# Kernel tuning notes

Measured on AMD Instinct MI355X. Metric: run time of the kernel, lower is better.

Reference implementation:

```python
import jax, jax.numpy as jnp
import numpy as np

NUM_HEADS = 16
D_MODEL = 2048
DUPLICATES = 4
DEPTH = D_MODEL // NUM_HEADS  # 128
KV_HEADS = NUM_HEADS // DUPLICATES  # 4


def rope(x):
    # x: (b, s, d); RoPE over first 2*(d//2) dims (d even here), as in source
    b, s, d = x.shape
    dim = d // 2
    inv_freq = (10000.0 ** (-jnp.arange(0, dim, dtype=jnp.float32) / dim)).astype(x.dtype)
    pos = jnp.arange(s, dtype=x.dtype)[None, :, None]  # (1, s, 1)
    freqs = pos * inv_freq  # (1, s, dim)
    cos, sin = jnp.cos(freqs), jnp.sin(freqs)
    x1, x2 = x[..., :dim], x[..., dim:]
    return jnp.concatenate([x1 * cos - x2 * sin, x2 * cos + x1 * sin], axis=-1)


def setup_inputs() -> dict:
    key = jax.random.key(0)
    ks = jax.random.split(key, 6)
    b, s = 2, 2048
    x = jax.random.normal(ks[0], (b, s, D_MODEL), dtype=jnp.float32)
    mask = jnp.ones((b, 1, s, s), dtype=bool)
    std = 0.02
    Wq = jax.random.normal(ks[1], (D_MODEL, D_MODEL), dtype=jnp.float32) * std
    Wk = jax.random.normal(ks[2], (D_MODEL, D_MODEL // DUPLICATES), dtype=jnp.float32) * std
    Wv = jax.random.normal(ks[3], (D_MODEL, D_MODEL // DUPLICATES), dtype=jnp.float32) * std
    Wo = jax.random.normal(ks[4], (D_MODEL, D_MODEL), dtype=jnp.float32) * std
    bo = jnp.zeros((1, 1, D_MODEL), dtype=jnp.float32)
    return {"x": x, "mask": mask, "Wq": Wq, "Wk": Wk, "Wv": Wv, "Wo": Wo, "bo": bo}


def reference(x, mask, Wq, Wk, Wv, Wo, bo):
    b, s, d = x.shape
    # QKV projections; RoPE applied on full projected vectors (as in source)
    q = rope(x @ Wq)          # (b, s, d_model)
    k = rope(x @ Wk)          # (b, s, d_model/dup)
    v = x @ Wv                # (b, s, d_model/dup)
    # split heads
    q = q.reshape(b, s, NUM_HEADS, DEPTH).transpose(0, 2, 1, 3)     # (b, H, s, depth)
    k = k.reshape(b, s, KV_HEADS, DEPTH).transpose(0, 2, 1, 3)      # (b, Hkv, s, depth)
    v = v.reshape(b, s, KV_HEADS, DEPTH).transpose(0, 2, 1, 3)
    # GQA repeat (jnp.repeat on head axis, matching source)
    k = jnp.repeat(k, DUPLICATES, axis=1)                            # (b, H, s, depth)
    v = jnp.repeat(v, DUPLICATES, axis=1)
    # scaled dot-product attention (chunking in source is a pure partition of q; math identical)
    logits = jnp.einsum('bhqd,bhkd->bhqk', q, k) / jnp.sqrt(jnp.asarray(DEPTH, x.dtype))
    logits = jnp.where(mask, logits, jnp.asarray(-1e9, x.dtype))
    attn = jax.nn.softmax(logits, axis=-1)
    out = jnp.einsum('bhqk,bhkd->bhqd', attn, v)                     # (b, H, s, depth)
    out = out.transpose(0, 2, 1, 3).reshape(b, s, d)
    return out @ Wo + bo
```

## Files before the change

kernel.cpp:

```cpp
#include <hip/hip_runtime.h>
#include <hip/hip_bf16.h>
#include <stdint.h>

#define NHEADS 16
#define KVHEADS 4
#define DEPTH 128
#define SEQ 2048
#define DM 2048
#define NQKV 3072
#define SCALE 0.08838834764831845f

using u16 = unsigned short;
using u32 = unsigned int;
using u64 = unsigned long long;
using bf16x8 = __attribute__((ext_vector_type(8))) __bf16;
using f32x4  = __attribute__((ext_vector_type(4))) float;
using f32x16 = __attribute__((ext_vector_type(16))) float;
using u32x4  = __attribute__((ext_vector_type(4))) u32;

__device__ __forceinline__ u16 bits(float f) {
  return __builtin_bit_cast(u16, (__bf16)f);
}
__device__ __forceinline__ u32 pk2(float a, float b) {
  return (u32)bits(a) | ((u32)bits(b) << 16);
}

__device__ __forceinline__ void gll16(const void* g, void* l) {
  __builtin_amdgcn_global_load_lds((const __attribute__((address_space(1))) void*)g,
                                   (__attribute__((address_space(3))) void*)l, 16, 0, 0);
}


__global__ void k_cvt_x(const float4* __restrict__ x, u16* __restrict__ o, int n4) {
  int i = blockIdx.x * 256 + threadIdx.x;
  if (i >= n4) return;
  float4 v = x[i];
  u64 pk = (u64)bits(v.x) | ((u64)bits(v.y) << 16) | ((u64)bits(v.z) << 32) | ((u64)bits(v.w) << 48);
  reinterpret_cast<u64*>(o)[i] = pk;
}

__global__ void k_transpose_w(const float* __restrict__ in, u16* __restrict__ out, int K, int N) {
  __shared__ float tile[32][33];
  int n0 = blockIdx.x * 32, k0 = blockIdx.y * 32;
  int tx = threadIdx.x, ty = threadIdx.y;
  for (int i = 0; i < 4; i++) tile[ty + i * 8][tx] = in[(size_t)(k0 + ty + i * 8) * N + n0 + tx];
  __syncthreads();
  for (int i = 0; i < 4; i++)
    out[(size_t)(n0 + ty + i * 8) * K + k0 + tx] = bits(tile[tx][ty + i * 8]);
}

__global__ void k_trig(float2* __restrict__ tab) {
  int idx = blockIdx.x * 256 + threadIdx.x;
  int s = idx >> 10, j = idx & 1023;
  float inv = expf((float)j * (-9.210340371976184f / 1024.f));
  float f = (float)s * inv;
  float sv, cv;
  sincosf(f, &sv, &cv);
  tab[idx] = make_float2(cv, sv);
}

__global__ void k_rope_q(const float* __restrict__ qkv, const float2* __restrict__ tab,
                         u16* __restrict__ Qh) {
  int idx = blockIdx.x * 256 + threadIdx.x;
  int col = idx & 2047;
  int row = idx >> 11;
  int s = row & 2047;
  const float* base = qkv + (size_t)row * NQKV;
  float v = base[col], out;
  if (col < 1024) {
    float2 cs = tab[s * 1024 + col];
    out = v * cs.x - base[col + 1024] * cs.y;
  } else {
    int j = col - 1024;
    float2 cs = tab[s * 1024 + j];
    out = v * cs.x + base[col - 1024] * cs.y;
  }
  int h = col >> 7, d = col & 127;
  Qh[(((size_t)(row >> 11) * NHEADS + h) * SEQ + s) * DEPTH + d] = bits(out * SCALE);
}

__global__ void k_rope_k(const float* __restrict__ qkv, const float2* __restrict__ tab,
                         u16* __restrict__ Kh) {
  int idx = blockIdx.x * 256 + threadIdx.x;
  int col = idx & 511;
  int row = idx >> 9;
  int s = row & 2047;
  const float* base = qkv + (size_t)row * NQKV + 2048;
  float v = base[col], out;
  if (col < 256) {
    float2 cs = tab[s * 1024 + col * 4];
    out = v * cs.x - base[col + 256] * cs.y;
  } else {
    int j = col - 256;
    float2 cs = tab[s * 1024 + j * 4];
    out = v * cs.x + base[col - 256] * cs.y;
  }
  int h = col >> 7, d = col & 127;
  Kh[(((size_t)(row >> 11) * KVHEADS + h) * SEQ + s) * DEPTH + d] = bits(out);
}

__global__ void k_transpose_v(const float* __restrict__ qkv, u16* __restrict__ Vt) {
  __shared__ float tile[32][33];
  int gy = blockIdx.y;
  int d0 = (gy & 3) * 32, kvh = (gy >> 2) & 3, b = gy >> 4;
  int s0 = blockIdx.x * 32;
  int tx = threadIdx.x, ty = threadIdx.y;
  const float* base = qkv + (size_t)b * SEQ * NQKV + 2560 + kvh * 128 + d0;
  for (int i = 0; i < 4; i++)
    tile[ty + i * 8][tx] = base[(size_t)(s0 + ty + i * 8) * NQKV + tx];
  __syncthreads();
  u16* obase = Vt + (((size_t)b * KVHEADS + kvh) * DEPTH + d0) * SEQ;
  for (int i = 0; i < 4; i++)
    obase[(size_t)(ty + i * 8) * SEQ + s0 + tx] = bits(tile[tx][ty + i * 8]);
}


#define GBAR __builtin_amdgcn_s_barrier()

#define GSTAGE(GBASE, LHALF, KT, ROWB) do {                                   \
  _Pragma("unroll") for (int i_ = 0; i_ < 2; i_++) {                          \
    int rl_ = (l >> 3) + w * 8 + i_ * 64;                                     \
    int cs_ = (l & 7) ^ ((rl_ & 4) >> 1);                                     \
    gll16((GBASE) + (size_t)((ROWB) + rl_) * K + (KT) * 64 + cs_ * 8,         \
          (char*)(LHALF) + w * 1024 + i_ * 8192);                             \
  }                                                                           \
} while (0)

#define LDA8(DB, MH) do {                                                     \
  const char* pa_ = (const char*)lA[DB][wm];                                  \
  _Pragma("unroll") for (int mi_ = 0; mi_ < 4; mi_++)                         \
  _Pragma("unroll") for (int kk_ = 0; kk_ < 2; kk_++) {                       \
    int row_ = (MH) * 64 + mi_ * 16 + lr;                                     \
    af[mi_ * 2 + kk_] = *(const bf16x8*)(pa_ + row_ * 128 +                   \
        (((kk_ * 4 + lg) ^ ((row_ & 4) >> 1)) * 16));                         \
  }                                                                           \
} while (0)

#define LDB4(DB, NH) do {                                                     \
  const char* pb_ = (const char*)lB[DB][wn >> 1];                             \
  _Pragma("unroll") for (int ni_ = 0; ni_ < 2; ni_++)                         \
  _Pragma("unroll") for (int kk_ = 0; kk_ < 2; kk_++) {                       \
    int row_ = (wn & 1) * 64 + (NH) * 32 + ni_ * 16 + lr;                     \
    bfr[ni_ * 2 + kk_] = *(const bf16x8*)(pb_ + row_ * 128 +                  \
        (((kk_ * 4 + lg) ^ ((row_ & 4) >> 1)) * 16));                         \
  }                                                                           \
} while (0)

#define PHASE_MFMA(MH, NH) do {                                               \
  __builtin_amdgcn_s_setprio(1);                                             \
  _Pragma("unroll") for (int mi_ = 0; mi_ < 4; mi_++)                         \
  _Pragma("unroll") for (int ni_ = 0; ni_ < 2; ni_++)                         \
  _Pragma("unroll") for (int kk_ = 0; kk_ < 2; kk_++)                         \
    acc[MH][NH][mi_][ni_] = __builtin_amdgcn_mfma_f32_16x16x32_bf16(          \
        af[mi_ * 2 + kk_], bfr[ni_ * 2 + kk_], acc[MH][NH][mi_][ni_], 0, 0, 0); \
  __builtin_amdgcn_s_setprio(0);                                             \
} while (0)

__global__ __launch_bounds__(512, 2) void k_gemm256(const u16* __restrict__ A,
                                                    const u16* __restrict__ B,
                                                    float* __restrict__ C, int M, int N, int K,
                                                    const float* __restrict__ bias) {
  __shared__ __align__(16) u16 lA[2][2][128 * 64];
  __shared__ __align__(16) u16 lB[2][2][128 * 64];
  int nt = N >> 8;
  int nwg = gridDim.x;
  int bid = blockIdx.x;
  int swz = (bid & 7) * (nwg >> 3) + (bid >> 3);
  int bm = swz / nt, bn = swz % nt;
  int tid = threadIdx.x;
  int w = tid >> 6, l = tid & 63;
  int lr = l & 15, lg = l >> 4;
  int wm = w >> 2, wn = w & 3;
  const u16* Abase = A + (size_t)(bm * 256) * K;
  const u16* Bbase = B + (size_t)(bn * 256) * K;
  int NT = K >> 6;

  f32x4 acc[2][2][4][2] = {};

  GSTAGE(Abase, lA[0][0], 0, 0);
  GSTAGE(Abase, lA[0][1], 0, 128);
  GSTAGE(Bbase, lB[0][0], 0, 0);
  GSTAGE(Bbase, lB[0][1], 0, 128);
  GSTAGE(Abase, lA[1][0], 1, 0);
  asm volatile("s_waitcnt vmcnt(2)" ::: "memory");
  GBAR;

  for (int j = 0; j < (NT >> 1); j++) {
    int kt1 = 2 * j + 1;
    int ktn0 = (2 * j + 2) & (NT - 1);
    int ktn1 = (2 * j + 3) & (NT - 1);
    bf16x8 af[8];
    bf16x8 bfr[4];
    LDA8(0, 0);
    LDB4(0, 0);
    GSTAGE(Abase, lA[1][1], kt1, 128);
    GBAR;
    PHASE_MFMA(0, 0);
    GBAR;
    LDB4(0, 1);
    GSTAGE(Bbase, lB[1][0], kt1, 0);
    GBAR;
    PHASE_MFMA(0, 1);
    GBAR;
    LDA8(0, 1);
    GSTAGE(Bbase, lB[1][1], kt1, 128);
    GBAR;
    PHASE_MFMA(1, 1);
    GBAR;
    LDB4(0, 0);
    GSTAGE(Abase, lA[0][0], ktn0, 0);
    asm volatile("s_waitcnt vmcnt(2)" ::: "memory");
    GBAR;
    PHASE_MFMA(1, 0);
    GBAR;
    LDA8(1, 0);
    LDB4(1, 0);
    GSTAGE(Abase, lA[0][1], ktn0, 128);
    GBAR;
    PHASE_MFMA(0, 0);
    GBAR;
    LDB4(1, 1);
    GSTAGE(Bbase, lB[0][0], ktn0, 0);
    GBAR;
    PHASE_MFMA(0, 1);
    GBAR;
    LDA8(1, 1);
    GSTAGE(Bbase, lB[0][1], ktn0, 128);
    GBAR;
    PHASE_MFMA(1, 1);
    GBAR;
    LDB4(1, 0);
    GSTAGE(Abase, lA[1][0], ktn1, 0);
    asm volatile("s_waitcnt vmcnt(2)" ::: "memory");
    GBAR;
    PHASE_MFMA(1, 0);
    GBAR;
  }
  asm volatile("s_waitcnt vmcnt(0)" ::: "memory");

  int r0 = bm * 256 + wm * 128, c0 = bn * 256 + wn * 64;
#pragma unroll
  for (int mh = 0; mh < 2; mh++)
#pragma unroll
    for (int mi = 0; mi < 4; mi++)
#pragma unroll
      for (int nh = 0; nh < 2; nh++)
#pragma unroll
        for (int ni = 0; ni < 2; ni++) {
          int col = c0 + nh * 32 + ni * 16 + lr;
          float bv = bias ? bias[col] : 0.f;
#pragma unroll
          for (int r = 0; r < 4; r++) {
            int row = r0 + mh * 64 + mi * 16 + lg * 4 + r;
            C[(size_t)row * N + col] = acc[mh][nh][mi][ni][r] + bv;
          }
        }
}

__global__ __launch_bounds__(256, 2) void k_attn(const u16* __restrict__ Qh,
                                                 const u16* __restrict__ Kh,
                                                 const u16* __restrict__ Vt,
                                                 u16* __restrict__ Ao) {
  __shared__ u16 lK[2][64 * 128];
  __shared__ u16 lV[2][128 * 64];
  __shared__ float lsc[4][32];

  int bid = blockIdx.x;
  int swz = (bid & 7) * 64 + (bid >> 3);
  int qt = swz & 15;
  int hd = (swz >> 4) & 3, kvh = (swz >> 6) & 3, b = swz >> 8;
  int h = kvh * 4 + hd;

  int tid = threadIdx.x;
  int w = tid >> 6, l = tid & 63;
  int hi = l >> 5;
  int q32 = l & 31;

  const u16* Kb = Kh + ((size_t)b * KVHEADS + kvh) * SEQ * DEPTH;
  const u16* Vb = Vt + ((size_t)b * KVHEADS + kvh) * DEPTH * SEQ;

  const u16* Qp = Qh + (((size_t)(b * NHEADS + h) * SEQ) + qt * 128 + w * 32 + q32) * DEPTH + hi * 8;
  bf16x8 qf[8];
#pragma unroll
  for (int ds = 0; ds < 8; ds++)
    qf[ds] = *reinterpret_cast<const bf16x8*>(Qp + ds * 16);

  f32x16 oacc[4] = {};
  float mrun = -INFINITY, lrun = 0.f;
  bool lo = (l < 32);

  {
#pragma unroll
    for (int i = 0; i < 4; i++) {
      int g = (w * 4 + i) * 64 + l;
      int kv = g >> 4, c = g & 15;
      gll16(Kb + (size_t)kv * DEPTH + ((c ^ (kv & 7)) << 3), (char*)lK[0] + (w * 4 + i) * 1024);
      int d = g >> 3, cv = g & 7;
      gll16(Vb + (size_t)d * SEQ + ((cv ^ (d & 7)) << 3), (char*)lV[0] + (w * 4 + i) * 1024);
    }
  }
  __syncthreads();

  int cur = 0;
  for (int t = 0; t < 32; t++) {
    if (t < 31) {
      int kv0 = (t + 1) * 64;
#pragma unroll
      for (int i = 0; i < 4; i++) {
        int g = (w * 4 + i) * 64 + l;
        int kv = g >> 4, c = g & 15;
        gll16(Kb + (size_t)(kv0 + kv) * DEPTH + ((c ^ (kv & 7)) << 3),
              (char*)lK[cur ^ 1] + (w * 4 + i) * 1024);
        int d = g >> 3, cv = g & 7;
        gll16(Vb + (size_t)d * SEQ + kv0 + ((cv ^ (d & 7)) << 3),
              (char*)lV[cur ^ 1] + (w * 4 + i) * 1024);
      }
    }

    const u16* lk = lK[cur];
    f32x16 sa[2] = {};
    __builtin_amdgcn_s_setprio(1);
#pragma unroll
    for (int ds = 0; ds < 8; ds++) {
#pragma unroll
      for (int a = 0; a < 2; a++) {
        int kv = a * 32 + q32;
        bf16x8 kf = *reinterpret_cast<const bf16x8*>(
            &lk[kv * DEPTH + (((ds * 2 + hi) ^ (kv & 7)) << 3)]);
        sa[a] = __builtin_amdgcn_mfma_f32_32x32x16_bf16(kf, qf[ds], sa[a], 0, 0, 0);
      }
    }
    __builtin_amdgcn_s_setprio(0);

    float pmax = sa[0][0];
#pragma unroll
    for (int r = 1; r < 16; r++) pmax = fmaxf(pmax, sa[0][r]);
#pragma unroll
    for (int r = 0; r < 16; r++) pmax = fmaxf(pmax, sa[1][r]);
    pmax = fmaxf(pmax, __shfl_xor(pmax, 32, 64));
    if (!__all(pmax - mrun <= 8.f)) {
      float mnew = fmaxf(mrun, pmax);
      float al = __expf(mrun - mnew);
      mrun = mnew;
      lrun *= al;
#pragma unroll
      for (int db = 0; db < 4; db++)
#pragma unroll
        for (int r = 0; r < 16; r++) oacc[db][r] *= al;
    }
    float ps = 0.f;
#pragma unroll
    for (int a = 0; a < 2; a++)
#pragma unroll
      for (int r = 0; r < 16; r++) {
        float p = __expf(sa[a][r] - mrun);
        sa[a][r] = p;
        ps += p;
      }
    ps += __shfl_xor(ps, 32, 64);
    lrun += ps;

    const u16* lv = lV[cur];
#pragma unroll
    for (int a = 0; a < 2; a++) {
#pragma unroll
      for (int js = 0; js < 2; js++) {
        int base = js * 8;
        u32 A0 = pk2(sa[a][base + 0], sa[a][base + 1]);
        u32 A1 = pk2(sa[a][base + 2], sa[a][base + 3]);
        u32 B0 = pk2(sa[a][base + 4], sa[a][base + 5]);
        u32 B1 = pk2(sa[a][base + 6], sa[a][base + 7]);
        asm volatile("v_permlane32_swap_b32 %0, %1" : "+v"(A0), "+v"(B0));
        asm volatile("v_permlane32_swap_b32 %0, %1" : "+v"(A1), "+v"(B1));
        u32x4 tw;
        tw.x = A0;
        tw.y = A1;
        tw.z = B0;
        tw.w = B1;
        bf16x8 pa = __builtin_bit_cast(bf16x8, tw);
        int ks = a * 2 + js;
        __builtin_amdgcn_s_setprio(1);
#pragma unroll
        for (int db = 0; db < 4; db++) {
          int d = db * 32 + q32;
          bf16x8 vf = *reinterpret_cast<const bf16x8*>(
              &lv[d * 64 + (((ks * 2 + hi) ^ (d & 7)) << 3)]);
          oacc[db] = __builtin_amdgcn_mfma_f32_32x32x16_bf16(pa, vf, oacc[db], 0, 0, 0);
        }
        __builtin_amdgcn_s_setprio(0);
      }
    }

    __syncthreads();
    cur ^= 1;
  }

  if (lo) lsc[w][q32] = 1.f / lrun;
  int q0 = qt * 128 + w * 32;
  u16* ob = Ao + (size_t)b * SEQ * DM + (size_t)h * DEPTH;
#pragma unroll
  for (int db = 0; db < 4; db++)
#pragma unroll
    for (int r = 0; r < 16; r++) {
      int row = (r & 3) + 8 * (r >> 2) + 4 * hi;
      ob[(size_t)(q0 + row) * DM + db * 32 + q32] = bits(oacc[db][r] * lsc[w][row]);
    }
}


extern "C" void kernel_launch(void* const* d_in, const int* in_sizes, int n_in,
                              void* d_out, int out_size, void* d_ws, size_t ws_size,
                              hipStream_t stream) {
  const float* x  = (const float*)d_in[0];
  const float* Wq = (const float*)d_in[2];
  const float* Wk = (const float*)d_in[3];
  const float* Wv = (const float*)d_in[4];
  const float* Wo = (const float*)d_in[5];
  const float* bo = (const float*)d_in[6];
  float* out = (float*)d_out;
  char* ws = (char*)d_ws;

  const size_t OFF_XB  = 0;
  const size_t OFF_WT  = 16777216;
  const size_t OFF_WOT = 29360128;
  const size_t OFF_TAB = 37748736;
  const size_t OFF_QKV = 54525952;
  const size_t OFF_QH  = 104857600;
  const size_t OFF_KH  = 121634816;
  const size_t OFF_VT  = 125829120;
  const size_t OFF_AO  = OFF_QKV;

  u16*    xb    = (u16*)(ws + OFF_XB);
  u16*    wqkvT = (u16*)(ws + OFF_WT);
  u16*    woT   = (u16*)(ws + OFF_WOT);
  float2* tab   = (float2*)(ws + OFF_TAB);
  float*  qkv   = (float*)(ws + OFF_QKV);
  u16*    Qhh   = (u16*)(ws + OFF_QH);
  u16*    Khh   = (u16*)(ws + OFF_KH);
  u16*    Vtt   = (u16*)(ws + OFF_VT);
  u16*    Ao    = (u16*)(ws + OFF_AO);

  dim3 tb(32, 8);
  k_cvt_x<<<8192, 256, 0, stream>>>((const float4*)x, xb, 2097152);
  k_transpose_w<<<dim3(64, 64), tb, 0, stream>>>(Wq, wqkvT, 2048, 2048);
  k_transpose_w<<<dim3(16, 64), tb, 0, stream>>>(Wk, wqkvT + (size_t)2048 * 2048, 2048, 512);
  k_transpose_w<<<dim3(16, 64), tb, 0, stream>>>(Wv, wqkvT + (size_t)2560 * 2048, 2048, 512);
  k_transpose_w<<<dim3(64, 64), tb, 0, stream>>>(Wo, woT, 2048, 2048);
  k_trig<<<8192, 256, 0, stream>>>(tab);
  k_gemm256<<<192, 512, 0, stream>>>(xb, wqkvT, qkv, 4096, 3072, 2048, nullptr);
  k_rope_q<<<32768, 256, 0, stream>>>(qkv, tab, Qhh);
  k_rope_k<<<8192, 256, 0, stream>>>(qkv, tab, Khh);
  k_transpose_v<<<dim3(64, 32), tb, 0, stream>>>(qkv, Vtt);
  k_attn<<<512, 256, 0, stream>>>(Qhh, Khh, Vtt, Ao);
  k_gemm256<<<128, 512, 0, stream>>>(Ao, woT, out, 4096, 2048, 2048, bo);
}
```

Before: 415.4 us.

## Pair GEMM global stages, widen K swizzle, use exp2 softmax with tree reductions

The GEMM main loop now issues the two halves of each A or B tile stage together and waits on vmcnt(4), which changes the prefetch schedule. The attention kernel widens the K LDS XOR swizzle from 8 to 16 chunks to reduce bank conflicts. Softmax folds log2(e) into the Q scale so it can use native exp2, with the rescale threshold adjusted to match. The row max and row sum become tree reductions instead of serial chains. These target load latency, LDS conflicts and the dependency chains in the softmax, at the cost of a different ordering of VMEM waits.

```diff
diff --git a/kernel.cpp b/kernel.cpp
--- a/kernel.cpp
+++ b/kernel.cpp
@@ -9,6 +9,8 @@
 #define DM 2048
 #define NQKV 3072
 #define SCALE 0.08838834764831845f
+#define LOG2E 1.4426950408889634f
+#define QSCL (SCALE * LOG2E)
 
 using u16 = unsigned short;
 using u32 = unsigned int;
@@ -23,6 +25,13 @@
 }
 __device__ __forceinline__ u32 pk2(float a, float b) {
   return (u32)bits(a) | ((u32)bits(b) << 16);
+}
+__device__ __forceinline__ float ex2(float x) {
+#if __has_builtin(__builtin_amdgcn_exp2f)
+  return __builtin_amdgcn_exp2f(x);
+#else
+  return exp2f(x);
+#endif
 }
 
 __device__ __forceinline__ void gll16(const void* g, void* l) {
@@ -76,7 +85,7 @@
     out = v * cs.x + base[col - 1024] * cs.y;
   }
   int h = col >> 7, d = col & 127;
-  Qh[(((size_t)(row >> 11) * NHEADS + h) * SEQ + s) * DEPTH + d] = bits(out * SCALE);
+  Qh[(((size_t)(row >> 11) * NHEADS + h) * SEQ + s) * DEPTH + d] = bits(out * QSCL);
 }
 
 __global__ void k_rope_k(const float* __restrict__ qkv, const float2* __restrict__ tab,
@@ -182,56 +191,57 @@
   GSTAGE(Bbase, lB[0][0], 0, 0);
   GSTAGE(Bbase, lB[0][1], 0, 128);
   GSTAGE(Abase, lA[1][0], 1, 0);
-  asm volatile("s_waitcnt vmcnt(2)" ::: "memory");
+  GSTAGE(Abase, lA[1][1], 1, 128);
+  asm volatile("s_waitcnt vmcnt(4)" ::: "memory");
   GBAR;
 
   for (int j = 0; j < (NT >> 1); j++) {
     int kt1 = 2 * j + 1;
-    int ktn0 = (2 * j + 2) & (NT - 1);
-    int ktn1 = (2 * j + 3) & (NT - 1);
+    int kt2 = (2 * j + 2) & (NT - 1);
+    int kt3 = (2 * j + 3) & (NT - 1);
     bf16x8 af[8];
     bf16x8 bfr[4];
     LDA8(0, 0);
     LDB4(0, 0);
-    GSTAGE(Abase, lA[1][1], kt1, 128);
+    GSTAGE(Bbase, lB[1][0], kt1, 0);
+    GSTAGE(Bbase, lB[1][1], kt1, 128);
     GBAR;
     PHASE_MFMA(0, 0);
     GBAR;
     LDB4(0, 1);
-    GSTAGE(Bbase, lB[1][0], kt1, 0);
     GBAR;
     PHASE_MFMA(0, 1);
     GBAR;
     LDA8(0, 1);
-    GSTAGE(Bbase, lB[1][1], kt1, 128);
     GBAR;
     PHASE_MFMA(1, 1);
     GBAR;
     LDB4(0, 0);
-    GSTAGE(Abase, lA[0][0], ktn0, 0);
-    asm volatile("s_waitcnt vmcnt(2)" ::: "memory");
+    GSTAGE(Abase, lA[0][0], kt2, 0);
+    GSTAGE(Abase, lA[0][1], kt2, 128);
+    asm volatile("s_waitcnt vmcnt(4)" ::: "memory");
     GBAR;
     PHASE_MFMA(1, 0);
     GBAR;
     LDA8(1, 0);
     LDB4(1, 0);
-    GSTAGE(Abase, lA[0][1], ktn0, 128);
+    GSTAGE(Bbase, lB[0][0], kt2, 0);
+    GSTAGE(Bbase, lB[0][1], kt2, 128);
     GBAR;
     PHASE_MFMA(0, 0);
     GBAR;
     LDB4(1, 1);
-    GSTAGE(Bbase, lB[0][0], ktn0, 0);
     GBAR;
     PHASE_MFMA(0, 1);
     GBAR;
     LDA8(1, 1);
-    GSTAGE(Bbase, lB[0][1], ktn0, 128);
     GBAR;
     PHASE_MFMA(1, 1);
     GBAR;
     LDB4(1, 0);
-    GSTAGE(Abase, lA[1][0], ktn1, 0);
-    asm volatile("s_waitcnt vmcnt(2)" ::: "memory");
+    GSTAGE(Abase, lA[1][0], kt3, 0);
+    GSTAGE(Abase, lA[1][1], kt3, 128);
+    asm volatile("s_waitcnt vmcnt(4)" ::: "memory");
     GBAR;
     PHASE_MFMA(1, 0);
     GBAR;
@@ -294,7 +304,7 @@
     for (int i = 0; i < 4; i++) {
       int g = (w * 4 + i) * 64 + l;
       int kv = g >> 4, c = g & 15;
-      gll16(Kb + (size_t)kv * DEPTH + ((c ^ (kv & 7)) << 3), (char*)lK[0] + (w * 4 + i) * 1024);
+      gll16(Kb + (size_t)kv * DEPTH + ((c ^ (kv & 15)) << 3), (char*)lK[0] + (w * 4 + i) * 1024);
       int d = g >> 3, cv = g & 7;
       gll16(Vb + (size_t)d * SEQ + ((cv ^ (d & 7)) << 3), (char*)lV[0] + (w * 4 + i) * 1024);
     }
@@ -309,7 +319,7 @@
       for (int i = 0; i < 4; i++) {
         int g = (w * 4 + i) * 64 + l;
         int kv = g >> 4, c = g & 15;
-        gll16(Kb + (size_t)(kv0 + kv) * DEPTH + ((c ^ (kv & 7)) << 3),
+        gll16(Kb + (size_t)(kv0 + kv) * DEPTH + ((c ^ (kv & 15)) << 3),
               (char*)lK[cur ^ 1] + (w * 4 + i) * 1024);
         int d = g >> 3, cv = g & 7;
         gll16(Vb + (size_t)d * SEQ + kv0 + ((cv ^ (d & 7)) << 3),
@@ -326,21 +336,24 @@
       for (int a = 0; a < 2; a++) {
         int kv = a * 32 + q32;
         bf16x8 kf = *reinterpret_cast<const bf16x8*>(
-            &lk[kv * DEPTH + (((ds * 2 + hi) ^ (kv & 7)) << 3)]);
+            &lk[kv * DEPTH + (((ds * 2 + hi) ^ (kv & 15)) << 3)]);
         sa[a] = __builtin_amdgcn_mfma_f32_32x32x16_bf16(kf, qf[ds], sa[a], 0, 0, 0);
       }
     }
     __builtin_amdgcn_s_setprio(0);
 
-    float pmax = sa[0][0];
-#pragma unroll
-    for (int r = 1; r < 16; r++) pmax = fmaxf(pmax, sa[0][r]);
-#pragma unroll
-    for (int r = 0; r < 16; r++) pmax = fmaxf(pmax, sa[1][r]);
-    pmax = fmaxf(pmax, __shfl_xor(pmax, 32, 64));
-    if (!__all(pmax - mrun <= 8.f)) {
+    float mx[16];
+#pragma unroll
+    for (int r = 0; r < 16; r++) mx[r] = fmaxf(sa[0][r], sa[1][r]);
+#pragma unroll
+    for (int s = 8; s > 0; s >>= 1)
+#pragma unroll
+      for (int r = 0; r < 16; r++)
+        if (r < s) mx[r] = fmaxf(mx[r], mx[r + s]);
+    float pmax = fmaxf(mx[0], __shfl_xor(mx[0], 32, 64));
+    if (!__all(pmax - mrun <= 11.54f)) {
       float mnew = fmaxf(mrun, pmax);
-      float al = __expf(mrun - mnew);
+      float al = ex2(mrun - mnew);
       mrun = mnew;
       lrun *= al;
 #pragma unroll
@@ -348,17 +361,21 @@
 #pragma unroll
         for (int r = 0; r < 16; r++) oacc[db][r] *= al;
     }
-    float ps = 0.f;
-#pragma unroll
-    for (int a = 0; a < 2; a++)
-#pragma unroll
-      for (int r = 0; r < 16; r++) {
-        float p = __expf(sa[a][r] - mrun);
-        sa[a][r] = p;
-        ps += p;
-      }
-    ps += __shfl_xor(ps, 32, 64);
-    lrun += ps;
+    float ss[16];
+#pragma unroll
+    for (int r = 0; r < 16; r++) {
+      float p0 = ex2(sa[0][r] - mrun);
+      float p1 = ex2(sa[1][r] - mrun);
+      sa[0][r] = p0;
+      sa[1][r] = p1;
+      ss[r] = p0 + p1;
+    }
+#pragma unroll
+    for (int s = 8; s > 0; s >>= 1)
+#pragma unroll
+      for (int r = 0; r < 16; r++)
+        if (r < s) ss[r] += ss[r + s];
+    lrun += ss[0] + __shfl_xor(ss[0], 32, 64);
 
     const u16* lv = lV[cur];
 #pragma unroll
```

Result: no change. 411.9 us (-0.8%).
